# Kernel tuning notes

Hardware: AMD Instinct MI355X
Metric: run time of the kernel (lower is better)

## Reference

```python
import jax, jax.numpy as jnp
import numpy as np

B, S, H = 8, 1024, 1536          # batch, seq, hidden_size
NH, HD, AH = 8, 96, 768          # heads after head_ratio=2, head_size=hidden/16, all_head_size
K = 7                            # conv_kernel_size
IM = 3072                        # intermediate_size
EPS = 1e-12                      # ConvBert layer_norm_eps


def _ln(x, g, b):
    m = x.mean(-1, keepdims=True)
    v = ((x - m) ** 2).mean(-1, keepdims=True)
    return (x - m) / jnp.sqrt(v + EPS) * g + b


def _windows(x, k):
    # x: [B,S,C] -> sliding windows [B,S,k,C] with 'same' padding ((k-1)//2 each side, k odd)
    p = (k - 1) // 2
    xp = jnp.pad(x, ((0, 0), (p, p), (0, 0)))
    idx = jnp.arange(x.shape[1])[:, None] + jnp.arange(k)[None, :]
    return xp[:, idx, :]


def _forward(embed, wq, bq, wk, bk, wv, bv, dw, pw, sep_b, wck, bck, wco, bco,
             wso, bso, ln1_g, ln1_b, wi, bi, wo, bo, ln2_g, ln2_b, wd, bd):
    b, s, _ = embed.shape
    # --- projections (weights stored [in,out]) ---
    q = embed @ wq + bq            # [B,S,AH]
    kk = embed @ wk + bk
    v = embed @ wv + bv
    # --- SeparableConv1D on hidden states: depthwise(k=7) then pointwise + bias ---
    win_h = _windows(embed, K)                             # [B,S,K,H]
    dconv = jnp.einsum('bskc,ck->bsc', win_h, dw)          # depthwise, [B,S,H]
    sep = dconv @ pw + sep_b                               # pointwise, [B,S,AH]
    # --- span dynamic conv kernels ---
    conv_attn = sep * q                                    # [B,S,AH]
    ck = (conv_attn @ wck + bck).reshape(b, s, NH, K)      # [B,S,NH,K]
    ck = jax.nn.softmax(ck, axis=-1)
    co = embed @ wco + bco                                 # [B,S,AH]
    win_co = _windows(co, K).reshape(b, s, K, NH, HD)      # [B,S,K,NH,HD]
    conv_out = jnp.einsum('bskhd,bshk->bshd', win_co, ck)  # [B,S,NH,HD]
    # --- standard self-attention on the reduced heads ---
    qh = q.reshape(b, s, NH, HD)
    kh = kk.reshape(b, s, NH, HD)
    vh = v.reshape(b, s, NH, HD)
    scores = jnp.einsum('bqhd,bkhd->bhqk', qh, kh) / jnp.sqrt(jnp.float32(HD))
    probs = jax.nn.softmax(scores, axis=-1)
    ctx = jnp.einsum('bhqk,bkhd->bqhd', probs, vh)         # [B,S,NH,HD]
    # --- concat attention heads with conv heads -> [B,S,2*NH,HD] -> [B,S,H] ---
    ctx = jnp.concatenate([ctx, conv_out], axis=2).reshape(b, s, H)
    # --- self output (dropout is identity at inference) ---
    attn_out = _ln(ctx @ wso + bso + embed, ln1_g, ln1_b)
    # --- FFN ---
    inter = jax.nn.gelu(attn_out @ wi + bi, approximate=False)
    layer_out = _ln(inter @ wo + bo + attn_out, ln2_g, ln2_b)
    # --- global max pooling over sequence + linear decoder ---
    pooled = layer_out.max(axis=1)                         # [B,H]
    logits = pooled @ wd + bd                              # [B,1]
    return logits


def setup_inputs() -> dict:
    key = jax.random.key(0)
    ks = jax.random.split(key, 32)
    rn = lambda i, shape, s=0.02: jax.random.normal(ks[i], shape, jnp.float32) * s
    d = {}
    d['embed'] = jax.random.normal(ks[0], (B, S, H), jnp.float32)
    d['wq'] = rn(1, (H, AH)); d['bq'] = jnp.zeros((AH,), jnp.float32)
    d['wk'] = rn(2, (H, AH)); d['bk'] = jnp.zeros((AH,), jnp.float32)
    d['wv'] = rn(3, (H, AH)); d['bv'] = jnp.zeros((AH,), jnp.float32)
    d['dw'] = rn(4, (H, K)); d['pw'] = rn(5, (H, AH)); d['sep_b'] = jnp.zeros((AH,), jnp.float32)
    d['wck'] = rn(6, (AH, NH * K)); d['bck'] = jnp.zeros((NH * K,), jnp.float32)
    d['wco'] = rn(7, (H, AH)); d['bco'] = jnp.zeros((AH,), jnp.float32)
    d['wso'] = rn(8, (H, H)); d['bso'] = jnp.zeros((H,), jnp.float32)
    d['ln1_g'] = jnp.ones((H,), jnp.float32); d['ln1_b'] = jnp.zeros((H,), jnp.float32)
    d['wi'] = rn(9, (H, IM)); d['bi'] = jnp.zeros((IM,), jnp.float32)
    d['wo'] = rn(10, (IM, H)); d['bo'] = jnp.zeros((H,), jnp.float32)
    d['ln2_g'] = jnp.ones((H,), jnp.float32); d['ln2_b'] = jnp.zeros((H,), jnp.float32)
    d['wd'] = jax.random.uniform(ks[11], (H, 1), jnp.float32, -0.1, 0.1)
    d['bd'] = jnp.zeros((1,), jnp.float32)
    return d


def reference(embed, wq, bq, wk, bk, wv, bv, dw, pw, sep_b, wck, bck, wco, bco,
              wso, bso, ln1_g, ln1_b, wi, bi, wo, bo, ln2_g, ln2_b, wd, bd):
    return _forward(embed, wq, bq, wk, bk, wv, bv, dw, pw, sep_b, wck, bck, wco, bco,
                    wso, bso, ln1_g, ln1_b, wi, bi, wo, bo, ln2_g, ln2_b, wd, bd)
```

## Files before the change

kernel.cpp:

```cpp
#include <hip/hip_runtime.h>


typedef __bf16 bf16_t;
typedef short s16x8 __attribute__((ext_vector_type(8)));
typedef float f32x4 __attribute__((ext_vector_type(4)));

#define BB  8
#define SS  1024
#define HH  1536
#define NHH 8
#define HDD 96
#define AHH 768
#define IMM 3072

__device__ __forceinline__ float rd_adapt(const void* p, long long i, int isbf) {
    return isbf ? (float)((const bf16_t*)p)[i] : ((const float*)p)[i];
}
__device__ __forceinline__ float bs2f(short x) {
    return __uint_as_float(((unsigned)(unsigned short)x) << 16);
}
__device__ __forceinline__ short f2bs(float f) {
    bf16_t b = (bf16_t)f; short s; __builtin_memcpy(&s, &b, 2); return s;
}

__device__ __forceinline__ float gelu_f(float v) {
    float u = v * (0.7978845608f + 0.0356774081f * v * v);
    float e = __expf(2.0f * u);
    float t = 1.0f - 2.0f / (e + 1.0f);
    return 0.5f * v * (1.0f + t);
}

__device__ __forceinline__ void gl2lds16(const bf16_t* g, bf16_t* l) {
    __builtin_amdgcn_global_load_lds(
        (__attribute__((address_space(1))) const void*)g,
        (__attribute__((address_space(3))) void*)l, 16, 0, 0);
}

#define FENCE() asm volatile("" ::: "memory")
#define BARRIER() do { FENCE(); __builtin_amdgcn_s_barrier(); FENCE(); } while (0)
#define LGKM(n) asm volatile("s_waitcnt lgkmcnt(" #n ")" ::: "memory")
#define VMCNT(n) asm volatile("s_waitcnt vmcnt(" #n ")" ::: "memory")
#define SCHEDB() __builtin_amdgcn_sched_barrier(0)
#define PRIO(n) __builtin_amdgcn_s_setprio(n)
#define RDV(base, imm) (*(const s16x8*)(smb + (base) + (imm)))

#define MFMA_CLUSTER(AF, BF, IO, JO)                                            \
    _Pragma("unroll")                                                           \
    for (int i_ = 0; i_ < 4; i_++)                                              \
        _Pragma("unroll")                                                       \
        for (int j_ = 0; j_ < 2; j_++) {                                        \
            acc[(IO)+i_][(JO)+j_] = __builtin_amdgcn_mfma_f32_16x16x32_bf16(    \
                AF[i_][0], BF[j_][0], acc[(IO)+i_][(JO)+j_], 0, 0, 0);          \
            acc[(IO)+i_][(JO)+j_] = __builtin_amdgcn_mfma_f32_16x16x32_bf16(    \
                AF[i_][1], BF[j_][1], acc[(IO)+i_][(JO)+j_], 0, 0, 0);          \
        }

__global__ __launch_bounds__(256)
void detect_kernel(const void* __restrict__ embed, int* __restrict__ flag)
{
    __shared__ int cnt[256];
    int t = threadIdx.x;
    float x = (float)((const bf16_t*)embed)[t];
    float a = fabsf(x);
    cnt[t] = (a > 1e-3f && a < 50.0f) ? 1 : 0;
    __syncthreads();
    for (int o = 128; o > 0; o >>= 1) { if (t < o) cnt[t] += cnt[t + o]; __syncthreads(); }
    if (t == 0) *flag = (cnt[0] >= 205) ? 1 : 0;
}

__global__ __launch_bounds__(256)
void convert_embed(const void* __restrict__ in, bf16_t* __restrict__ out,
                   const int* __restrict__ flagp)
{
    int isbf = *flagp;
    long long i0 = ((long long)blockIdx.x * 256 + threadIdx.x) * 8;
    if (isbf) {
        *(s16x8*)(out + i0) = *(const s16x8*)((const bf16_t*)in + i0);
    } else {
        const float* f = (const float*)in;
        #pragma unroll
        for (int j = 0; j < 8; j++) out[i0 + j] = (bf16_t)f[i0 + j];
    }
}

__global__ __launch_bounds__(256)
void concat_bias(const void* __restrict__ b0, const void* __restrict__ b1,
                 const void* __restrict__ b2, const void* __restrict__ b3,
                 bf16_t* __restrict__ out, const int* __restrict__ flagp)
{
    int isbf = *flagp;
    int t = blockIdx.x * 256 + threadIdx.x;
    int sel = t / 768, off = t - sel * 768;
    const void* src = (sel == 0) ? b0 : (sel == 1) ? b1 : (sel == 2) ? b2 : b3;
    out[t] = (bf16_t)rd_adapt(src, off, isbf);
}

__global__ __launch_bounds__(256)
void dw_transpose(const void* __restrict__ dw, float* __restrict__ dwT,
                  const int* __restrict__ flagp)
{
    int isbf = *flagp;
    int i = blockIdx.x * 256 + threadIdx.x;
    if (i >= 7 * HH) return;
    int k = i % 7, c = i / 7;
    dwT[k * HH + c] = rd_adapt(dw, (long long)c * 7 + k, isbf);
}

template<int IB, int OB>
__device__ __forceinline__ void tile_step(
    char* smb, int vA0, int vA1, int vB0, int vB1,
    const char* gA00, const char* gA01, const char* gA10, const char* gA11,
    const char* gB00, const char* gB01, const char* gB10, const char* gB11,
    char* ldsAw, char* ldsBw, int k1, int k2,
    s16x8 (&af0)[4][2], s16x8 (&af1)[4][2],
    s16x8 (&bf0)[2][2], s16x8 (&bf1)[2][2],
    f32x4 (&acc)[8][4])
{
    BARRIER();
    bf1[0][0] = RDV(vB0, IB + 4096); bf1[0][1] = RDV(vB1, IB + 4096);
    bf1[1][0] = RDV(vB0, IB + 6144); bf1[1][1] = RDV(vB1, IB + 6144);
    gl2lds16((const bf16_t*)(gA10 + k1), (bf16_t*)(ldsAw + OB + 16384));
    gl2lds16((const bf16_t*)(gA11 + k1), (bf16_t*)(ldsAw + OB + 17408));
    LGKM(4); SCHEDB(); PRIO(1);
    MFMA_CLUSTER(af0, bf0, 0, 0);
    PRIO(0);

    BARRIER();
    af1[0][0] = RDV(vA0, IB + 8192);  af1[0][1] = RDV(vA1, IB + 8192);
    af1[1][0] = RDV(vA0, IB + 10240); af1[1][1] = RDV(vA1, IB + 10240);
    af1[2][0] = RDV(vA0, IB + 12288); af1[2][1] = RDV(vA1, IB + 12288);
    af1[3][0] = RDV(vA0, IB + 14336); af1[3][1] = RDV(vA1, IB + 14336);
    gl2lds16((const bf16_t*)(gB10 + k1), (bf16_t*)(ldsBw + OB + 16384));
    gl2lds16((const bf16_t*)(gB11 + k1), (bf16_t*)(ldsBw + OB + 17408));
    LGKM(8); SCHEDB(); PRIO(1);
    MFMA_CLUSTER(af0, bf1, 0, 2);
    PRIO(0);

    BARRIER();
    gl2lds16((const bf16_t*)(gB00 + k2), (bf16_t*)(ldsBw + IB));
    gl2lds16((const bf16_t*)(gB01 + k2), (bf16_t*)(ldsBw + IB + 1024));
    gl2lds16((const bf16_t*)(gA00 + k2), (bf16_t*)(ldsAw + IB));
    gl2lds16((const bf16_t*)(gA01 + k2), (bf16_t*)(ldsAw + IB + 1024));
    LGKM(0); SCHEDB(); PRIO(1);
    MFMA_CLUSTER(af1, bf1, 4, 2);
    PRIO(0);

    VMCNT(4);
    BARRIER();
    af0[0][0] = RDV(vA0, OB + 0);    af0[0][1] = RDV(vA1, OB + 0);
    af0[1][0] = RDV(vA0, OB + 2048); af0[1][1] = RDV(vA1, OB + 2048);
    af0[2][0] = RDV(vA0, OB + 4096); af0[2][1] = RDV(vA1, OB + 4096);
    af0[3][0] = RDV(vA0, OB + 6144); af0[3][1] = RDV(vA1, OB + 6144);
    PRIO(1);
    MFMA_CLUSTER(af1, bf0, 4, 0);
    PRIO(0);
    bf0[0][0] = RDV(vB0, OB + 0);    bf0[0][1] = RDV(vB1, OB + 0);
    bf0[1][0] = RDV(vB0, OB + 2048); bf0[1][1] = RDV(vB1, OB + 2048);
}

__global__ __launch_bounds__(512, 2)
void gemm256(const bf16_t* __restrict__ A, const bf16_t* __restrict__ Bt,
             bf16_t* __restrict__ C, const void* __restrict__ bias,
             const bf16_t* __restrict__ emul, int lde, const int* __restrict__ flagp,
             int M, int N, int Kd, int lda, int ldb, int ldc, int act, int tilesN)
{
    __shared__ bf16_t Sm[65536];
    char* smb = (char*)Sm;
    int isbf = flagp ? *flagp : 1;

    int nwg = gridDim.x;
    int orig = blockIdx.x;
    int q = nwg >> 3, r = nwg & 7;
    int xcd = orig & 7, lid = orig >> 3;
    int wg = (xcd < r ? xcd * (q + 1) : r * (q + 1) + (xcd - r) * q) + lid;
    int row0 = (wg / tilesN) * 256;
    int col0 = (wg % tilesN) * 256;

    int tid = threadIdx.x;
    int wave = tid >> 6, lane = tid & 63;
    int wm = wave >> 2, wn = wave & 3;
    int lm = lane & 15, kq = lane >> 4;

    int srow = lane >> 3;
    int scol = 8 * ((lane & 7) ^ srow);

    const char* gA00 = (const char*)(A + (long long)(row0 +   0 + (2*wave + 0)*8 + srow) * lda + scol);
    const char* gA01 = (const char*)(A + (long long)(row0 +   0 + (2*wave + 1)*8 + srow) * lda + scol);
    const char* gA10 = (const char*)(A + (long long)(row0 + 128 + (2*wave + 0)*8 + srow) * lda + scol);
    const char* gA11 = (const char*)(A + (long long)(row0 + 128 + (2*wave + 1)*8 + srow) * lda + scol);
    const char* gB00 = (const char*)(Bt + (long long)(col0 +   0 + (2*wave + 0)*8 + srow) * ldb + scol);
    const char* gB01 = (const char*)(Bt + (long long)(col0 +   0 + (2*wave + 1)*8 + srow) * ldb + scol);
    const char* gB10 = (const char*)(Bt + (long long)(col0 + 128 + (2*wave + 0)*8 + srow) * ldb + scol);
    const char* gB11 = (const char*)(Bt + (long long)(col0 + 128 + (2*wave + 1)*8 + srow) * ldb + scol);

    char* ldsAw = smb + 2 * wave * 1024;
    char* ldsBw = smb + 65536 + 2 * wave * 1024;

    int xo = (lm & 7) << 4;
    int c0 = (kq * 16) ^ xo;
    int c1 = (64 + kq * 16) ^ xo;
    int vA0 = (wm * 128 + lm) * 128 + c0;
    int vA1 = (wm * 128 + lm) * 128 + c1;
    int vB0 = 65536 + (wn * 64 + lm) * 128 + c0;
    int vB1 = 65536 + (wn * 64 + lm) * 128 + c1;

    f32x4 acc[8][4] = {};
    s16x8 af0[4][2], af1[4][2], bf0[2][2], bf1[2][2];

    int KT = Kd >> 6;
    int KTm1 = KT - 1;

    gl2lds16((const bf16_t*)gA00, (bf16_t*)(ldsAw));
    gl2lds16((const bf16_t*)gA01, (bf16_t*)(ldsAw + 1024));
    gl2lds16((const bf16_t*)gA10, (bf16_t*)(ldsAw + 16384));
    gl2lds16((const bf16_t*)gA11, (bf16_t*)(ldsAw + 17408));
    gl2lds16((const bf16_t*)gB00, (bf16_t*)(ldsBw));
    gl2lds16((const bf16_t*)gB01, (bf16_t*)(ldsBw + 1024));
    gl2lds16((const bf16_t*)gB10, (bf16_t*)(ldsBw + 16384));
    gl2lds16((const bf16_t*)gB11, (bf16_t*)(ldsBw + 17408));
    int kb1 = min(1, KTm1) << 7;
    gl2lds16((const bf16_t*)(gB00 + kb1), (bf16_t*)(ldsBw + 32768));
    gl2lds16((const bf16_t*)(gB01 + kb1), (bf16_t*)(ldsBw + 33792));
    gl2lds16((const bf16_t*)(gA00 + kb1), (bf16_t*)(ldsAw + 32768));
    gl2lds16((const bf16_t*)(gA01 + kb1), (bf16_t*)(ldsAw + 33792));
    VMCNT(4);
    BARRIER();
    af0[0][0] = RDV(vA0, 0);    af0[0][1] = RDV(vA1, 0);
    af0[1][0] = RDV(vA0, 2048); af0[1][1] = RDV(vA1, 2048);
    af0[2][0] = RDV(vA0, 4096); af0[2][1] = RDV(vA1, 4096);
    af0[3][0] = RDV(vA0, 6144); af0[3][1] = RDV(vA1, 6144);
    bf0[0][0] = RDV(vB0, 0);    bf0[0][1] = RDV(vB1, 0);
    bf0[1][0] = RDV(vB0, 2048); bf0[1][1] = RDV(vB1, 2048);

    for (int it = 0; it < (KT >> 1); ++it) {
        int t = it << 1;
        int k1 = min(t + 1, KTm1) << 7;
        int k2 = min(t + 2, KTm1) << 7;
        int k3 = min(t + 3, KTm1) << 7;
        tile_step<0, 32768>(smb, vA0, vA1, vB0, vB1,
                            gA00, gA01, gA10, gA11, gB00, gB01, gB10, gB11,
                            ldsAw, ldsBw, k1, k2, af0, af1, bf0, bf1, acc);
        tile_step<32768, 0>(smb, vA0, vA1, vB0, vB1,
                            gA00, gA01, gA10, gA11, gB00, gB01, gB10, gB11,
                            ldsAw, ldsBw, k2, k3, af0, af1, bf0, bf1, acc);
    }

    #pragma unroll
    for (int j = 0; j < 4; j++) {
        int gcol = col0 + wn * 64 + j * 16 + lm;
        float bv = bias ? rd_adapt(bias, gcol, isbf) : 0.0f;
        #pragma unroll
        for (int ip = 0; ip < 8; ip++) {
            int grow0 = row0 + wm * 128 + ip * 16 + kq * 4;
            #pragma unroll
            for (int r = 0; r < 4; r++) {
                float v = acc[ip][j][r] + bv;
                if (emul) v *= (float)emul[(long long)(grow0 + r) * lde + gcol];
                if (act) v = gelu_f(v);
                C[(long long)(grow0 + r) * ldc + gcol] = (bf16_t)v;
            }
        }
    }
}

__global__ __launch_bounds__(256)
void gemm_tile(const bf16_t* __restrict__ A, const bf16_t* __restrict__ Bt,
               bf16_t* __restrict__ C, const void* __restrict__ bias, long long biasOff,
               const bf16_t* __restrict__ emul, int lde, const int* __restrict__ flagp,
               int M, int N, int Kd, int lda, int ldb, int ldc,
               float scale, int act, int beta, int nlim)
{
    __shared__ bf16_t Sm[16384];

    int isbf = flagp ? *flagp : 1;
    int tid  = threadIdx.x;
    int wave = tid >> 6, lane = tid & 63;
    int wm = wave >> 1, wn = wave & 1;
    int row0 = blockIdx.x * 128;
    int col0 = blockIdx.y * 128;
    int lm = lane & 15;
    int kq = lane >> 4;

    int sr = tid >> 2;
    int sc = (tid & 3) * 8;
    const bf16_t* ga0 = A + (long long)(row0 + sr) * lda + sc;
    const bf16_t* ga1 = A + (long long)(row0 + 64 + sr) * lda + sc;
    int br0 = min(col0 + sr, nlim);
    int br1 = min(col0 + 64 + sr, nlim);
    const bf16_t* gb0 = Bt + (long long)br0 * ldb + sc;
    const bf16_t* gb1 = Bt + (long long)br1 * ldb + sc;
    bf16_t* lw = Sm + wave * 512;

    f32x4 acc[4][4] = {};

    for (int k0 = 0; k0 < Kd; k0 += 64) {
        #pragma unroll
        for (int h = 0; h < 2; h++) {
            int kh = k0 + h * 32;
            gl2lds16(ga0 + kh, lw + h * 4096);
            gl2lds16(ga1 + kh, lw + h * 4096 + 2048);
            gl2lds16(gb0 + kh, lw + 8192 + h * 4096);
            gl2lds16(gb1 + kh, lw + 8192 + h * 4096 + 2048);
        }
        __syncthreads();

        s16x8 af[2][4], bfr[2][4];
        #pragma unroll
        for (int h = 0; h < 2; h++) {
            #pragma unroll
            for (int i = 0; i < 4; i++)
                af[h][i] = *(const s16x8*)(Sm + h * 4096 + (wm * 64 + i * 16 + lm) * 32 + kq * 8);
            #pragma unroll
            for (int j = 0; j < 4; j++)
                bfr[h][j] = *(const s16x8*)(Sm + 8192 + h * 4096 + (wn * 64 + j * 16 + lm) * 32 + kq * 8);
        }
        #pragma unroll
        for (int i = 0; i < 4; i++)
            #pragma unroll
            for (int j = 0; j < 4; j++) {
                acc[i][j] = __builtin_amdgcn_mfma_f32_16x16x32_bf16(af[0][i], bfr[0][j], acc[i][j], 0, 0, 0);
                acc[i][j] = __builtin_amdgcn_mfma_f32_16x16x32_bf16(af[1][i], bfr[1][j], acc[i][j], 0, 0, 0);
            }
        __syncthreads();
    }

    #pragma unroll
    for (int j = 0; j < 4; j++) {
        int gcol = col0 + wn * 64 + j * 16 + lm;
        if (gcol >= N) continue;
        float bv = bias ? rd_adapt(bias, biasOff + gcol, isbf) : 0.0f;
        #pragma unroll
        for (int i = 0; i < 4; i++) {
            int grow0 = row0 + wm * 64 + i * 16 + kq * 4;
            #pragma unroll
            for (int r = 0; r < 4; r++) {
                float v = acc[i][j][r] * scale + bv;
                long long ci = (long long)(grow0 + r) * ldc + gcol;
                if (beta) v += (float)C[ci];
                if (emul) v *= (float)emul[(long long)(grow0 + r) * lde + gcol];
                if (act) v = gelu_f(v);
                C[ci] = (bf16_t)v;
            }
        }
    }
}

__global__ __launch_bounds__(256, 2)
void flash_attn(const bf16_t* __restrict__ qkv, const bf16_t* __restrict__ vT,
                bf16_t* __restrict__ ctxcat)
{
    const float ascale = 0.1020620726159658f;
    __shared__ bf16_t KL[12288];
    __shared__ bf16_t Pl[4 * 32 * 136];

    int bh = blockIdx.x;
    int b = bh >> 3, h = bh & 7;
    const bf16_t* Qp = qkv  + (long long)b * SS * 3072 + h * HDD;
    const bf16_t* Kp = qkv  + (long long)b * SS * 3072 + 768 + h * HDD;
    const bf16_t* Vt = vT   + (long long)b * AHH * SS + (long long)h * HDD * SS;
    bf16_t*       Op = ctxcat + (long long)b * SS * HH + h * HDD;

    int tid = threadIdx.x, wave = tid >> 6, lane = tid & 63;
    int lm = lane & 15, kq = lane >> 4;
    int q0 = blockIdx.y * 128 + wave * 32;
    bf16_t* Pw = Pl + wave * 32 * 136;

    int srow_l = lane >> 2;
    int sslot  = ((lane & 3) ^ ((lane >> 3) & 3)) * 8;
    auto stageK = [&](int kt) {
        #pragma unroll
        for (int i = 0; i < 6; i++) {
            int qc = wave + 4 * i;
            int fb = qc >> 3, cc = qc & 7;
            gl2lds16(Kp + (long long)(kt * 128 + cc * 16 + srow_l) * 3072 + fb * 32 + sslot,
                     KL + qc * 512);
        }
    };
    const char* klb = (const char*)KL + lm * 64 + ((kq ^ ((lm >> 1) & 3)) << 4);

    s16x8 aq[2][3];
    #pragma unroll
    for (int i = 0; i < 2; i++)
        #pragma unroll
        for (int kf = 0; kf < 3; kf++)
            aq[i][kf] = *(const s16x8*)(Qp + (long long)(q0 + i * 16 + lm) * 3072 + kf * 32 + kq * 8);

    stageK(0);
    __syncthreads();

    f32x4 Oacc[2][6] = {};
    float mrow[2][4], lrow[2][4];
    #pragma unroll
    for (int i = 0; i < 2; i++)
        #pragma unroll
        for (int r = 0; r < 4; r++) { mrow[i][r] = -1e30f; lrow[i][r] = 0.0f; }

    for (int kt = 0; kt < 8; kt++) {
        f32x4 S[2][8] = {};
        #pragma unroll
        for (int j = 0; j < 8; j++) {
            s16x8 bk[3];
            #pragma unroll
            for (int kf = 0; kf < 3; kf++)
                bk[kf] = *(const s16x8*)(klb + kf * 8192 + j * 1024);
            #pragma unroll
            for (int i = 0; i < 2; i++)
                #pragma unroll
                for (int kf = 0; kf < 3; kf++)
                    S[i][j] = __builtin_amdgcn_mfma_f32_16x16x32_bf16(aq[i][kf], bk[kf], S[i][j], 0, 0, 0);
        }
        __syncthreads();
        if (kt < 7) stageK(kt + 1);

        float mnew[2][4];
        #pragma unroll
        for (int i = 0; i < 2; i++) {
            #pragma unroll
            for (int r = 0; r < 4; r++) {
                float mx = -1e30f;
                #pragma unroll
                for (int j = 0; j < 8; j++) mx = fmaxf(mx, S[i][j][r]);
                #pragma unroll
                for (int msk = 1; msk <= 8; msk <<= 1) mx = fmaxf(mx, __shfl_xor(mx, msk));
                mnew[i][r] = fmaxf(mrow[i][r], mx * ascale);
            }
        }
        #pragma unroll
        for (int i = 0; i < 2; i++) {
            #pragma unroll
            for (int r = 0; r < 4; r++) {
                float al = __expf(mrow[i][r] - mnew[i][r]);
                lrow[i][r] *= al;
                #pragma unroll
                for (int n = 0; n < 6; n++) Oacc[i][n][r] *= al;
                mrow[i][r] = mnew[i][r];
            }
        }
        float psum[2][4] = {};
        #pragma unroll
        for (int i = 0; i < 2; i++) {
            #pragma unroll
            for (int j = 0; j < 8; j++) {
                #pragma unroll
                for (int r = 0; r < 4; r++) {
                    float p = __expf(S[i][j][r] * ascale - mnew[i][r]);
                    psum[i][r] += p;
                    Pw[(i * 16 + kq * 4 + r) * 136 + j * 16 + lm] = (bf16_t)p;
                }
            }
        }
        #pragma unroll
        for (int i = 0; i < 2; i++) {
            #pragma unroll
            for (int r = 0; r < 4; r++) {
                float t = psum[i][r];
                #pragma unroll
                for (int msk = 1; msk <= 8; msk <<= 1) t += __shfl_xor(t, msk);
                lrow[i][r] += t;
            }
        }

        s16x8 ap[2][4];
        #pragma unroll
        for (int i = 0; i < 2; i++)
            #pragma unroll
            for (int kf = 0; kf < 4; kf++)
                ap[i][kf] = *(const s16x8*)(Pw + (i * 16 + lm) * 136 + kf * 32 + kq * 8);
        #pragma unroll
        for (int n = 0; n < 6; n++) {
            s16x8 bv[4];
            #pragma unroll
            for (int kf = 0; kf < 4; kf++)
                bv[kf] = *(const s16x8*)(Vt + (long long)(n * 16 + lm) * SS + kt * 128 + kf * 32 + kq * 8);
            #pragma unroll
            for (int i = 0; i < 2; i++)
                #pragma unroll
                for (int kf = 0; kf < 4; kf++)
                    Oacc[i][n] = __builtin_amdgcn_mfma_f32_16x16x32_bf16(ap[i][kf], bv[kf], Oacc[i][n], 0, 0, 0);
        }
        __syncthreads();
    }

    #pragma unroll
    for (int i = 0; i < 2; i++) {
        #pragma unroll
        for (int n = 0; n < 6; n++) {
            #pragma unroll
            for (int r = 0; r < 4; r++) {
                int row = q0 + i * 16 + kq * 4 + r;
                int col = n * 16 + lm;
                Op[(long long)row * HH + col] = (bf16_t)(Oacc[i][n][r] / lrow[i][r]);
            }
        }
    }
}

__global__ __launch_bounds__(256)
void transpose_v8(const void* __restrict__ in, bf16_t* __restrict__ out,
                  int R, int C, int ldin, long long inOff,
                  long long sInB, long long sOutB, const int* __restrict__ flagp)
{
    __shared__ bf16_t t[64][72];
    int isbf = flagp ? *flagp : 1;
    int z = blockIdx.z;
    long long base = inOff + (long long)z * sInB;
    bf16_t* op = out + (long long)z * sOutB;
    int cb = blockIdx.x * 64, rb = blockIdx.y * 64;
    int tr = threadIdx.x >> 3;
    int tc = (threadIdx.x & 7) * 8;
    #pragma unroll
    for (int it = 0; it < 2; it++) {
        int r = tr + it * 32;
        int gc = cb + tc;
        if (isbf && gc + 8 <= C) {
            *(s16x8*)&t[r][tc] =
                *(const s16x8*)((const bf16_t*)in + base + (long long)(rb + r) * ldin + gc);
        } else {
            #pragma unroll
            for (int j = 0; j < 8; j++)
                t[r][tc + j] = (gc + j < C)
                    ? (bf16_t)rd_adapt(in, base + (long long)(rb + r) * ldin + gc + j, isbf)
                    : (bf16_t)0.0f;
        }
    }
    __syncthreads();
    int oc = threadIdx.x >> 2;
    int r0 = (threadIdx.x & 3) * 16;
    s16x8 v0, v1;
    #pragma unroll
    for (int j = 0; j < 8; j++) v0[j] = f2bs(bs2f(*(short*)&t[r0 + j][oc]));
    #pragma unroll
    for (int j = 0; j < 8; j++) v1[j] = f2bs(bs2f(*(short*)&t[r0 + 8 + j][oc]));
    bf16_t* dst = op + (long long)(cb + oc) * R + rb + r0;
    *(s16x8*)dst = v0;
    *(s16x8*)(dst + 8) = v1;
}

__global__ __launch_bounds__(256)
void transpose_pad4(const void* __restrict__ i0, const void* __restrict__ i1,
                    const void* __restrict__ i2, const void* __restrict__ i3,
                    bf16_t* __restrict__ out, const int* __restrict__ flagp)
{
    __shared__ bf16_t t[64][72];
    int isbf = *flagp;
    int z = blockIdx.z;
    const void* in = (z == 0) ? i0 : (z == 1) ? i1 : (z == 2) ? i2 : i3;
    bf16_t* op = out + (long long)z * (768ll * 1536);
    int cb = blockIdx.x * 64, rb = blockIdx.y * 64;
    int tr = threadIdx.x >> 3;
    int tc = (threadIdx.x & 7) * 8;
    #pragma unroll
    for (int it = 0; it < 2; it++) {
        int r = tr + it * 32;
        if (isbf) {
            *(s16x8*)&t[r][tc] =
                *(const s16x8*)((const bf16_t*)in + (long long)(rb + r) * 768 + cb + tc);
        } else {
            #pragma unroll
            for (int j = 0; j < 8; j++)
                t[r][tc + j] = (bf16_t)rd_adapt(in, (long long)(rb + r) * 768 + cb + tc + j, isbf);
        }
    }
    __syncthreads();
    int oc = threadIdx.x >> 2;
    int r0 = (threadIdx.x & 3) * 16;
    s16x8 v0, v1;
    #pragma unroll
    for (int j = 0; j < 8; j++) v0[j] = *(short*)&t[r0 + j][oc];
    #pragma unroll
    for (int j = 0; j < 8; j++) v1[j] = *(short*)&t[r0 + 8 + j][oc];
    bf16_t* dst = op + (long long)(cb + oc) * 1536 + rb + r0;
    *(s16x8*)dst = v0;
    *(s16x8*)(dst + 8) = v1;
}

__global__ __launch_bounds__(256)
void dconv_kernel(const bf16_t* __restrict__ ebuf, const float* __restrict__ dwT,
                  bf16_t* __restrict__ out)
{
    long long i = (long long)blockIdx.x * 256 + threadIdx.x;
    int c8 = (int)(i % 192) * 8;
    long long bs = i / 192;
    int s = (int)(bs % SS);
    float acc[8] = {};
    #pragma unroll
    for (int k = 0; k < 7; k++) {
        int ss = s + k - 3;
        if (ss < 0 || ss >= SS) continue;
        s16x8 v = *(const s16x8*)(ebuf + (bs + (k - 3)) * HH + c8);
        const float4* wp = (const float4*)(dwT + k * HH + c8);
        float4 w0 = wp[0], w1 = wp[1];
        acc[0] += bs2f(v[0]) * w0.x; acc[1] += bs2f(v[1]) * w0.y;
        acc[2] += bs2f(v[2]) * w0.z; acc[3] += bs2f(v[3]) * w0.w;
        acc[4] += bs2f(v[4]) * w1.x; acc[5] += bs2f(v[5]) * w1.y;
        acc[6] += bs2f(v[6]) * w1.z; acc[7] += bs2f(v[7]) * w1.w;
    }
    s16x8 o;
    #pragma unroll
    for (int j = 0; j < 8; j++) o[j] = f2bs(acc[j]);
    *(s16x8*)(out + bs * HH + c8) = o;
}

__global__ __launch_bounds__(256)
void ck_softmax(const bf16_t* __restrict__ ck, float* __restrict__ ckp)
{
    int i = blockIdx.x * 256 + threadIdx.x;
    if (i >= BB * SS * NHH) return;
    int h = i % NHH;
    long long bs = i / NHH;
    const bf16_t* src = ck + bs * 64 + h * 7;
    float v[7], mx = -1e30f;
    #pragma unroll
    for (int k = 0; k < 7; k++) { v[k] = (float)src[k]; mx = fmaxf(mx, v[k]); }
    float sum = 0.0f;
    #pragma unroll
    for (int k = 0; k < 7; k++) { v[k] = expf(v[k] - mx); sum += v[k]; }
    float inv = 1.0f / sum;
    float* dst = ckp + bs * 56 + h * 7;
    #pragma unroll
    for (int k = 0; k < 7; k++) dst[k] = v[k] * inv;
}

__global__ __launch_bounds__(256)
void conv_out_kernel(const bf16_t* __restrict__ co, int ldco,
                     const float* __restrict__ ckp, bf16_t* __restrict__ ctxcat)
{
    long long i = (long long)blockIdx.x * 256 + threadIdx.x;
    int ch = (int)(i % 96);
    long long bs = i / 96;
    int s = (int)(bs % SS);
    int hd0 = ch * 8;
    int h = hd0 / HDD;
    const float* w = ckp + bs * 56 + h * 7;
    float wk[7];
    #pragma unroll
    for (int k = 0; k < 7; k++) wk[k] = w[k];
    float acc[8] = {};
    #pragma unroll
    for (int k = 0; k < 7; k++) {
        int ss = s + k - 3;
        if (ss < 0 || ss >= SS) continue;
        s16x8 v = *(const s16x8*)(co + (bs + (k - 3)) * ldco + hd0);
        #pragma unroll
        for (int j = 0; j < 8; j++) acc[j] += bs2f(v[j]) * wk[k];
    }
    s16x8 o;
    #pragma unroll
    for (int j = 0; j < 8; j++) o[j] = f2bs(acc[j]);
    *(s16x8*)(ctxcat + bs * HH + AHH + hd0) = o;
}

__global__ __launch_bounds__(192)
void ln_kernel(const bf16_t* __restrict__ y, const bf16_t* __restrict__ res,
               const void* __restrict__ g, const void* __restrict__ bta,
               bf16_t* __restrict__ outb, const int* __restrict__ flagp)
{
    int isbf = *flagp;
    long long row = blockIdx.x;
    int tid = threadIdx.x;
    int c0 = tid * 8;
    s16x8 vy = *(const s16x8*)(y + row * HH + c0);
    s16x8 vr = *(const s16x8*)(res + row * HH + c0);
    float x[8], s = 0.0f, s2 = 0.0f;
    #pragma unroll
    for (int j = 0; j < 8; j++) {
        float v = bs2f(vy[j]) + bs2f(vr[j]);
        x[j] = v; s += v; s2 += v * v;
    }
    #pragma unroll
    for (int o = 32; o > 0; o >>= 1) { s += __shfl_down(s, o); s2 += __shfl_down(s2, o); }
    __shared__ float w1[3], w2[3];
    int lane = tid & 63, wv = tid >> 6;
    if (lane == 0) { w1[wv] = s; w2[wv] = s2; }
    __syncthreads();
    float S1 = w1[0] + w1[1] + w1[2];
    float S2 = w2[0] + w2[1] + w2[2];
    float mean = S1 * (1.0f / HH);
    float var  = S2 * (1.0f / HH) - mean * mean;
    float inv  = rsqrtf(var + 1e-12f);
    s16x8 o;
    #pragma unroll
    for (int j = 0; j < 8; j++) {
        float v = (x[j] - mean) * inv * rd_adapt(g, c0 + j, isbf) + rd_adapt(bta, c0 + j, isbf);
        o[j] = f2bs(v);
    }
    *(s16x8*)(outb + row * HH + c0) = o;
}

__global__ __launch_bounds__(192)
void maxpool_p1(const bf16_t* __restrict__ lo, float* __restrict__ part)
{
    int sc = blockIdx.x, b = blockIdx.y;
    int tid = threadIdx.x;
    int c0 = tid * 8;
    const bf16_t* p = lo + ((long long)b * SS + sc * 32) * HH + c0;
    float m[8];
    #pragma unroll
    for (int j = 0; j < 8; j++) m[j] = -1e30f;
    for (int r = 0; r < 32; r++) {
        s16x8 v = *(const s16x8*)(p + (long long)r * HH);
        #pragma unroll
        for (int j = 0; j < 8; j++) m[j] = fmaxf(m[j], bs2f(v[j]));
    }
    float* dst = part + ((long long)b * 32 + sc) * HH + c0;
    *(float4*)(dst)     = make_float4(m[0], m[1], m[2], m[3]);
    *(float4*)(dst + 4) = make_float4(m[4], m[5], m[6], m[7]);
}

__global__ __launch_bounds__(192)
void pool_decode(const float* __restrict__ part, const void* __restrict__ wd,
                 const void* __restrict__ bd, void* __restrict__ out,
                 const int* __restrict__ flagp)
{
    int isbf = *flagp;
    int b = blockIdx.x;
    int tid = threadIdx.x;
    int c0 = tid * 8;
    float m[8];
    #pragma unroll
    for (int j = 0; j < 8; j++) m[j] = -1e30f;
    for (int ch = 0; ch < 32; ch++) {
        const float4* q = (const float4*)(part + ((long long)b * 32 + ch) * HH + c0);
        float4 a = q[0], c = q[1];
        m[0] = fmaxf(m[0], a.x); m[1] = fmaxf(m[1], a.y);
        m[2] = fmaxf(m[2], a.z); m[3] = fmaxf(m[3], a.w);
        m[4] = fmaxf(m[4], c.x); m[5] = fmaxf(m[5], c.y);
        m[6] = fmaxf(m[6], c.z); m[7] = fmaxf(m[7], c.w);
    }
    float s = 0.0f;
    #pragma unroll
    for (int j = 0; j < 8; j++) s += m[j] * rd_adapt(wd, c0 + j, isbf);
    #pragma unroll
    for (int o = 32; o > 0; o >>= 1) s += __shfl_down(s, o);
    __shared__ float sa[3];
    int lane = tid & 63, wv = tid >> 6;
    if (lane == 0) sa[wv] = s;
    __syncthreads();
    if (tid == 0) {
        float r = sa[0] + sa[1] + sa[2] + rd_adapt(bd, 0, isbf);
        if (isbf) ((bf16_t*)out)[b] = (bf16_t)r;
        else      ((float*)out)[b]  = r;
    }
}

extern "C" void kernel_launch(void* const* d_in, const int* in_sizes, int n_in,
                              void* d_out, int out_size, void* d_ws, size_t ws_size,
                              hipStream_t stream)
{
    const void* embed = d_in[0];
    const void* wq  = d_in[1];  const void* bq  = d_in[2];
    const void* wk  = d_in[3];  const void* bk  = d_in[4];
    const void* wv  = d_in[5];  const void* bv  = d_in[6];
    const void* dw  = d_in[7];  const void* pw  = d_in[8];  const void* sep_b = d_in[9];
    const void* wck = d_in[10]; const void* bck = d_in[11];
    const void* wco = d_in[12]; const void* bco = d_in[13];
    const void* wso = d_in[14]; const void* bso = d_in[15];
    const void* ln1g = d_in[16]; const void* ln1b = d_in[17];
    const void* wi  = d_in[18]; const void* bi  = d_in[19];
    const void* wo  = d_in[20]; const void* bo  = d_in[21];
    const void* ln2g = d_in[22]; const void* ln2b = d_in[23];
    const void* wd  = d_in[24]; const void* bd  = d_in[25];
    (void)ws_size; (void)in_sizes; (void)n_in; (void)out_size;

    char* ws = (char*)d_ws;
    char* A  = ws;
    char* B  = ws + 50331648;
    char* C_ = ws + 75497472;
    char* D  = ws + 88080384;
    char* E  = ws + 113246208;
    char* F  = ws + 138412032;
    char* XP = ws + 143130624;

    bf16_t* qkvco  = (bf16_t*)A;
    bf16_t* ybuf   = (bf16_t*)A;
    bf16_t* interb = (bf16_t*)A;
    bf16_t* lout   = (bf16_t*)A;
    bf16_t* wT_all = (bf16_t*)B;
    bf16_t* dconvb = (bf16_t*)B;
    bf16_t* ckb    = (bf16_t*)B;
    float*  ckp    = (float*)(B + 1310720);
    bf16_t* vT     = (bf16_t*)B;
    bf16_t* wfT    = (bf16_t*)B;
    bf16_t* sepb   = (bf16_t*)C_;
    float*  mpart  = (float*)C_;
    bf16_t* ctxcat = (bf16_t*)D;
    bf16_t* attn   = (bf16_t*)D;
    bf16_t* ebuf   = (bf16_t*)E;
    bf16_t* y2     = (bf16_t*)E;
    bf16_t* wT     = (bf16_t*)F;
    int*    flag   = (int*)XP;
    bf16_t* cbias  = (bf16_t*)(XP + 256);
    float*  dwT    = (float*)(XP + 8192);

    dim3 blk(256);

    auto gemm_big = [&](const bf16_t* Ai, const bf16_t* Bt, bf16_t* Ci, const void* bias,
                        const bf16_t* emul, int lde, const int* fl,
                        int M, int N, int Kd, int lda, int ldb, int ldc, int act) {
        int tn = N / 256;
        dim3 g((M / 256) * tn);
        gemm256<<<g, dim3(512), 0, stream>>>(Ai, Bt, Ci, bias, emul, lde, fl,
                                             M, N, Kd, lda, ldb, ldc, act, tn);
    };
    auto gemm = [&](const bf16_t* Ai, const bf16_t* Bt, bf16_t* Ci, const void* bias,
                    long long biasOff, const bf16_t* emul, int lde, const int* fl,
                    int M, int N, int Kd, int lda, int ldb, int ldc,
                    float scale, int act, int beta, int nlim) {
        dim3 g(M / 128, (N + 127) / 128, 1);
        gemm_tile<<<g, blk, 0, stream>>>(Ai, Bt, Ci, bias, biasOff, emul, lde, fl,
                                         M, N, Kd, lda, ldb, ldc,
                                         scale, act, beta, nlim);
    };
    auto transpose = [&](const void* in, bf16_t* out, int R, int Cc, int Cpad, int ldin,
                         long long inOff, int batch, long long sInB, long long sOutB,
                         const int* fl) {
        dim3 g(Cpad / 64, R / 64, batch);
        transpose_v8<<<g, blk, 0, stream>>>(in, out, R, Cc, ldin, inOff, sInB, sOutB, fl);
    };

    detect_kernel<<<dim3(1), blk, 0, stream>>>(embed, flag);
    convert_embed<<<dim3(6144), blk, 0, stream>>>(embed, ebuf, flag);

    transpose_pad4<<<dim3(12, 24, 4), blk, 0, stream>>>(wq, wk, wv, wco, wT_all, flag);
    concat_bias<<<dim3(12), blk, 0, stream>>>(bq, bk, bv, bco, cbias, flag);
    gemm_big(ebuf, wT_all, qkvco, cbias, nullptr, 0, nullptr,
             8192, 3072, 1536, HH, HH, 3072, 0);

    dw_transpose<<<dim3(42), blk, 0, stream>>>(dw, dwT, flag);
    dconv_kernel<<<dim3((BB * SS * 192) / 256), blk, 0, stream>>>(ebuf, dwT, dconvb);
    transpose(pw, wT, 1536, 768, 768, 768, 0, 1, 0, 0, flag);
    gemm(dconvb, wT, sepb, sep_b, 0, qkvco, 3072, flag,
         8192, 768, 1536, HH, HH, AHH, 1.0f, 0, 0, 767);

    transpose(wck, wT, 768, 56, 128, 56, 0, 1, 0, 0, flag);
    gemm(sepb, wT, ckb, bck, 0, nullptr, 0, flag,
         8192, 56, 768, AHH, AHH, 64, 1.0f, 0, 0, 127);
    ck_softmax<<<dim3((BB * SS * NHH) / 256), blk, 0, stream>>>(ckb, ckp);
    conv_out_kernel<<<dim3((BB * SS * 96) / 256), blk, 0, stream>>>(qkvco + 2304, 3072, ckp, ctxcat);

    transpose(qkvco, vT, 1024, 768, 768, 3072, 1536, 8, 1024ll * 3072, 768ll * 1024, nullptr);
    flash_attn<<<dim3(64, 8), blk, 0, stream>>>(qkvco, vT, ctxcat);

    transpose(wso, wT, 1536, 1536, 1536, 1536, 0, 1, 0, 0, flag);
    gemm_big(ctxcat, wT, ybuf, bso, nullptr, 0, flag,
             8192, 1536, 1536, HH, HH, HH, 0);
    ln_kernel<<<dim3(8192), dim3(192), 0, stream>>>(ybuf, ebuf, ln1g, ln1b, attn, flag);

    transpose(wi, wfT, 1536, 3072, 3072, 3072, 0, 1, 0, 0, flag);
    gemm_big(attn, wfT, interb, bi, nullptr, 0, flag,
             8192, 3072, 1536, HH, HH, IMM, 1);
    transpose(wo, wfT, 3072, 1536, 1536, 1536, 0, 1, 0, 0, flag);
    gemm_big(interb, wfT, y2, bo, nullptr, 0, flag,
             8192, 1536, 3072, IMM, IMM, HH, 0);
    ln_kernel<<<dim3(8192), dim3(192), 0, stream>>>(y2, attn, ln2g, ln2b, lout, flag);

    maxpool_p1<<<dim3(32, 8), dim3(192), 0, stream>>>(lout, mpart);
    pool_decode<<<dim3(BB), dim3(192), 0, stream>>>(mpart, wd, bd, d_out, flag);
}
```

Before: 847.2 us.

## Batch weight prep into two kernels, fuse softmax and residual adds

```diff
diff --git a/kernel.cpp b/kernel.cpp
--- a/kernel.cpp
+++ b/kernel.cpp
@@ -83,27 +83,96 @@
     }
 }
 
+__device__ __forceinline__ void tr64_body(const void* in, bf16_t* out,
+                                          int C, int ldin, int R,
+                                          int cb, int rb, int isbf,
+                                          bf16_t (*t)[72])
+{
+    int tr = threadIdx.x >> 3;
+    int tc = (threadIdx.x & 7) * 8;
+    #pragma unroll
+    for (int it = 0; it < 2; it++) {
+        int r = tr + it * 32;
+        int gc = cb + tc;
+        if (isbf && gc + 8 <= C) {
+            *(s16x8*)&t[r][tc] =
+                *(const s16x8*)((const bf16_t*)in + (long long)(rb + r) * ldin + gc);
+        } else {
+            #pragma unroll
+            for (int j = 0; j < 8; j++)
+                t[r][tc + j] = (gc + j < C)
+                    ? (bf16_t)rd_adapt(in, (long long)(rb + r) * ldin + gc + j, isbf)
+                    : (bf16_t)0.0f;
+        }
+    }
+    __syncthreads();
+    int oc = threadIdx.x >> 2;
+    int r0 = (threadIdx.x & 3) * 16;
+    s16x8 v0, v1;
+    #pragma unroll
+    for (int j = 0; j < 8; j++) v0[j] = *(short*)&t[r0 + j][oc];
+    #pragma unroll
+    for (int j = 0; j < 8; j++) v1[j] = *(short*)&t[r0 + 8 + j][oc];
+    bf16_t* dst = out + (long long)(cb + oc) * R + rb + r0;
+    *(s16x8*)dst = v0;
+    *(s16x8*)(dst + 8) = v1;
+}
+
 __global__ __launch_bounds__(256)
-void concat_bias(const void* __restrict__ b0, const void* __restrict__ b1,
-                 const void* __restrict__ b2, const void* __restrict__ b3,
-                 bf16_t* __restrict__ out, const int* __restrict__ flagp)
-{
+void prep_weights(const void* __restrict__ wq, const void* __restrict__ wk,
+                  const void* __restrict__ wv, const void* __restrict__ wco,
+                  const void* __restrict__ pw, const void* __restrict__ wck,
+                  const void* __restrict__ dw,
+                  const void* __restrict__ b0, const void* __restrict__ b1,
+                  const void* __restrict__ b2, const void* __restrict__ b3,
+                  bf16_t* __restrict__ wT_all, bf16_t* __restrict__ pwT,
+                  bf16_t* __restrict__ wckT, float* __restrict__ dwT,
+                  bf16_t* __restrict__ cbias, const int* __restrict__ flagp)
+{
+    __shared__ bf16_t t[64][72];
     int isbf = *flagp;
-    int t = blockIdx.x * 256 + threadIdx.x;
-    int sel = t / 768, off = t - sel * 768;
-    const void* src = (sel == 0) ? b0 : (sel == 1) ? b1 : (sel == 2) ? b2 : b3;
-    out[t] = (bf16_t)rd_adapt(src, off, isbf);
+    int j = blockIdx.x;
+    if (j < 1152) {
+        int z = j / 288, rm = j % 288;
+        const void* in = (z == 0) ? wq : (z == 1) ? wk : (z == 2) ? wv : wco;
+        tr64_body(in, wT_all + (long long)z * 768 * 1536, 768, 768, 1536,
+                  (rm % 12) * 64, (rm / 12) * 64, isbf, t);
+    } else if (j < 1440) {
+        int rm = j - 1152;
+        tr64_body(pw, pwT, 768, 768, 1536, (rm % 12) * 64, (rm / 12) * 64, isbf, t);
+    } else if (j < 1464) {
+        int rm = j - 1440;
+        tr64_body(wck, wckT, 56, 56, 768, (rm % 2) * 64, (rm / 2) * 64, isbf, t);
+    } else if (j < 1506) {
+        int idx = (j - 1464) * 256 + threadIdx.x;
+        int k = idx % 7, c = idx / 7;
+        dwT[k * HH + c] = rd_adapt(dw, (long long)c * 7 + k, isbf);
+    } else {
+        int tt = (j - 1506) * 256 + threadIdx.x;
+        int sel = tt / 768, off = tt - sel * 768;
+        const void* src = (sel == 0) ? b0 : (sel == 1) ? b1 : (sel == 2) ? b2 : b3;
+        cbias[tt] = (bf16_t)rd_adapt(src, off, isbf);
+    }
 }
 
 __global__ __launch_bounds__(256)
-void dw_transpose(const void* __restrict__ dw, float* __restrict__ dwT,
-                  const int* __restrict__ flagp)
-{
+void prep_late(const void* __restrict__ wso, const void* __restrict__ wi,
+               const void* __restrict__ wo, bf16_t* __restrict__ wsoT,
+               bf16_t* __restrict__ wiT, bf16_t* __restrict__ woT,
+               const int* __restrict__ flagp)
+{
+    __shared__ bf16_t t[64][72];
     int isbf = *flagp;
-    int i = blockIdx.x * 256 + threadIdx.x;
-    if (i >= 7 * HH) return;
-    int k = i % 7, c = i / 7;
-    dwT[k * HH + c] = rd_adapt(dw, (long long)c * 7 + k, isbf);
+    int j = blockIdx.x;
+    if (j < 576) {
+        tr64_body(wso, wsoT, 1536, 1536, 1536, (j % 24) * 64, (j / 24) * 64, isbf, t);
+    } else if (j < 1728) {
+        int rm = j - 576;
+        tr64_body(wi, wiT, 3072, 3072, 1536, (rm % 48) * 64, (rm / 48) * 64, isbf, t);
+    } else {
+        int rm = j - 1728;
+        tr64_body(wo, woT, 1536, 1536, 3072, (rm % 24) * 64, (rm / 24) * 64, isbf, t);
+    }
 }
 
 template<int IB, int OB>
@@ -161,6 +230,7 @@
 __global__ __launch_bounds__(512, 2)
 void gemm256(const bf16_t* __restrict__ A, const bf16_t* __restrict__ Bt,
              bf16_t* __restrict__ C, const void* __restrict__ bias,
+             const bf16_t* __restrict__ resi, int ldr,
              const bf16_t* __restrict__ emul, int lde, const int* __restrict__ flagp,
              int M, int N, int Kd, int lda, int ldb, int ldc, int act, int tilesN)
 {
@@ -255,6 +325,7 @@
             #pragma unroll
             for (int r = 0; r < 4; r++) {
                 float v = acc[ip][j][r] + bv;
+                if (resi) v += (float)resi[(long long)(grow0 + r) * ldr + gcol];
                 if (emul) v *= (float)emul[(long long)(grow0 + r) * lde + gcol];
                 if (act) v = gelu_f(v);
                 C[(long long)(grow0 + r) * ldc + gcol] = (bf16_t)v;
@@ -528,48 +599,10 @@
     int r0 = (threadIdx.x & 3) * 16;
     s16x8 v0, v1;
     #pragma unroll
-    for (int j = 0; j < 8; j++) v0[j] = f2bs(bs2f(*(short*)&t[r0 + j][oc]));
-    #pragma unroll
-    for (int j = 0; j < 8; j++) v1[j] = f2bs(bs2f(*(short*)&t[r0 + 8 + j][oc]));
+    for (int j = 0; j < 8; j++) v0[j] = *(short*)&t[r0 + j][oc];
+    #pragma unroll
+    for (int j = 0; j < 8; j++) v1[j] = *(short*)&t[r0 + 8 + j][oc];
     bf16_t* dst = op + (long long)(cb + oc) * R + rb + r0;
-    *(s16x8*)dst = v0;
-    *(s16x8*)(dst + 8) = v1;
-}
-
-__global__ __launch_bounds__(256)
-void transpose_pad4(const void* __restrict__ i0, const void* __restrict__ i1,
-                    const void* __restrict__ i2, const void* __restrict__ i3,
-                    bf16_t* __restrict__ out, const int* __restrict__ flagp)
-{
-    __shared__ bf16_t t[64][72];
-    int isbf = *flagp;
-    int z = blockIdx.z;
-    const void* in = (z == 0) ? i0 : (z == 1) ? i1 : (z == 2) ? i2 : i3;
-    bf16_t* op = out + (long long)z * (768ll * 1536);
-    int cb = blockIdx.x * 64, rb = blockIdx.y * 64;
-    int tr = threadIdx.x >> 3;
-    int tc = (threadIdx.x & 7) * 8;
-    #pragma unroll
-    for (int it = 0; it < 2; it++) {
-        int r = tr + it * 32;
-        if (isbf) {
-            *(s16x8*)&t[r][tc] =
-                *(const s16x8*)((const bf16_t*)in + (long long)(rb + r) * 768 + cb + tc);
-        } else {
-            #pragma unroll
-            for (int j = 0; j < 8; j++)
-                t[r][tc + j] = (bf16_t)rd_adapt(in, (long long)(rb + r) * 768 + cb + tc + j, isbf);
-        }
-    }
-    __syncthreads();
-    int oc = threadIdx.x >> 2;
-    int r0 = (threadIdx.x & 3) * 16;
-    s16x8 v0, v1;
-    #pragma unroll
-    for (int j = 0; j < 8; j++) v0[j] = *(short*)&t[r0 + j][oc];
-    #pragma unroll
-    for (int j = 0; j < 8; j++) v1[j] = *(short*)&t[r0 + 8 + j][oc];
-    bf16_t* dst = op + (long long)(cb + oc) * 1536 + rb + r0;
     *(s16x8*)dst = v0;
     *(s16x8*)(dst + 8) = v1;
 }
@@ -602,28 +635,8 @@
 }
 
 __global__ __launch_bounds__(256)
-void ck_softmax(const bf16_t* __restrict__ ck, float* __restrict__ ckp)
-{
-    int i = blockIdx.x * 256 + threadIdx.x;
-    if (i >= BB * SS * NHH) return;
-    int h = i % NHH;
-    long long bs = i / NHH;
-    const bf16_t* src = ck + bs * 64 + h * 7;
-    float v[7], mx = -1e30f;
-    #pragma unroll
-    for (int k = 0; k < 7; k++) { v[k] = (float)src[k]; mx = fmaxf(mx, v[k]); }
-    float sum = 0.0f;
-    #pragma unroll
-    for (int k = 0; k < 7; k++) { v[k] = expf(v[k] - mx); sum += v[k]; }
-    float inv = 1.0f / sum;
-    float* dst = ckp + bs * 56 + h * 7;
-    #pragma unroll
-    for (int k = 0; k < 7; k++) dst[k] = v[k] * inv;
-}
-
-__global__ __launch_bounds__(256)
 void conv_out_kernel(const bf16_t* __restrict__ co, int ldco,
-                     const float* __restrict__ ckp, bf16_t* __restrict__ ctxcat)
+                     const bf16_t* __restrict__ ckb, bf16_t* __restrict__ ctxcat)
 {
     long long i = (long long)blockIdx.x * 256 + threadIdx.x;
     int ch = (int)(i % 96);
@@ -631,10 +644,17 @@
     int s = (int)(bs % SS);
     int hd0 = ch * 8;
     int h = hd0 / HDD;
-    const float* w = ckp + bs * 56 + h * 7;
-    float wk[7];
-    #pragma unroll
-    for (int k = 0; k < 7; k++) wk[k] = w[k];
+    const bf16_t* src = ckb + bs * 64 + h * 7;
+    float wk[7], mx = -1e30f;
+    #pragma unroll
+    for (int k = 0; k < 7; k++) { wk[k] = (float)src[k]; mx = fmaxf(mx, wk[k]); }
+    float sum = 0.0f;
+    #pragma unroll
+    for (int k = 0; k < 7; k++) { wk[k] = expf(wk[k] - mx); sum += wk[k]; }
+    float inv = 1.0f / sum;
+    #pragma unroll
+    for (int k = 0; k < 7; k++) wk[k] *= inv;
+
     float acc[8] = {};
     #pragma unroll
     for (int k = 0; k < 7; k++) {
@@ -651,7 +671,7 @@
 }
 
 __global__ __launch_bounds__(192)
-void ln_kernel(const bf16_t* __restrict__ y, const bf16_t* __restrict__ res,
+void ln_kernel(const bf16_t* __restrict__ y,
                const void* __restrict__ g, const void* __restrict__ bta,
                bf16_t* __restrict__ outb, const int* __restrict__ flagp)
 {
@@ -660,11 +680,10 @@
     int tid = threadIdx.x;
     int c0 = tid * 8;
     s16x8 vy = *(const s16x8*)(y + row * HH + c0);
-    s16x8 vr = *(const s16x8*)(res + row * HH + c0);
     float x[8], s = 0.0f, s2 = 0.0f;
     #pragma unroll
     for (int j = 0; j < 8; j++) {
-        float v = bs2f(vy[j]) + bs2f(vr[j]);
+        float v = bs2f(vy[j]);
         x[j] = v; s += v; s2 += v * v;
     }
     #pragma unroll
@@ -778,16 +797,18 @@
     bf16_t* wT_all = (bf16_t*)B;
     bf16_t* dconvb = (bf16_t*)B;
     bf16_t* ckb    = (bf16_t*)B;
-    float*  ckp    = (float*)(B + 1310720);
     bf16_t* vT     = (bf16_t*)B;
-    bf16_t* wfT    = (bf16_t*)B;
+    bf16_t* wiT    = (bf16_t*)B;
+    bf16_t* woT    = (bf16_t*)(B + 9437184);
     bf16_t* sepb   = (bf16_t*)C_;
     float*  mpart  = (float*)C_;
     bf16_t* ctxcat = (bf16_t*)D;
     bf16_t* attn   = (bf16_t*)D;
     bf16_t* ebuf   = (bf16_t*)E;
     bf16_t* y2     = (bf16_t*)E;
-    bf16_t* wT     = (bf16_t*)F;
+    bf16_t* pwT    = (bf16_t*)F;
+    bf16_t* wckT   = (bf16_t*)(F + 2359296);
+    bf16_t* wsoT   = (bf16_t*)F;
     int*    flag   = (int*)XP;
     bf16_t* cbias  = (bf16_t*)(XP + 256);
     float*  dwT    = (float*)(XP + 8192);
@@ -795,11 +816,12 @@
     dim3 blk(256);
 
     auto gemm_big = [&](const bf16_t* Ai, const bf16_t* Bt, bf16_t* Ci, const void* bias,
-                        const bf16_t* emul, int lde, const int* fl,
-                        int M, int N, int Kd, int lda, int ldb, int ldc, int act) {
+                        const bf16_t* resi, int ldr, const bf16_t* emul, int lde,
+                        const int* fl, int M, int N, int Kd, int lda, int ldb, int ldc,
+                        int act) {
         int tn = N / 256;
         dim3 g((M / 256) * tn);
-        gemm256<<<g, dim3(512), 0, stream>>>(Ai, Bt, Ci, bias, emul, lde, fl,
+        gemm256<<<g, dim3(512), 0, stream>>>(Ai, Bt, Ci, bias, resi, ldr, emul, lde, fl,
                                              M, N, Kd, lda, ldb, ldc, act, tn);
     };
     auto gemm = [&](const bf16_t* Ai, const bf16_t* Bt, bf16_t* Ci, const void* bias,
@@ -811,48 +833,39 @@
                                          M, N, Kd, lda, ldb, ldc,
                                          scale, act, beta, nlim);
     };
-    auto transpose = [&](const void* in, bf16_t* out, int R, int Cc, int Cpad, int ldin,
-                         long long inOff, int batch, long long sInB, long long sOutB,
-                         const int* fl) {
-        dim3 g(Cpad / 64, R / 64, batch);
-        transpose_v8<<<g, blk, 0, stream>>>(in, out, R, Cc, ldin, inOff, sInB, sOutB, fl);
-    };
 
     detect_kernel<<<dim3(1), blk, 0, stream>>>(embed, flag);
+    prep_weights<<<dim3(1518), blk, 0, stream>>>(wq, wk, wv, wco, pw, wck, dw,
+                                                 bq, bk, bv, bco,
+                                                 wT_all, pwT, wckT, dwT, cbias, flag);
     convert_embed<<<dim3(6144), blk, 0, stream>>>(embed, ebuf, flag);
 
-    transpose_pad4<<<dim3(12, 24, 4), blk, 0, stream>>>(wq, wk, wv, wco, wT_all, flag);
-    concat_bias<<<dim3(12), blk, 0, stream>>>(bq, bk, bv, bco, cbias, flag);
-    gemm_big(ebuf, wT_all, qkvco, cbias, nullptr, 0, nullptr,
+    gemm_big(ebuf, wT_all, qkvco, cbias, nullptr, 0, nullptr, 0, nullptr,
              8192, 3072, 1536, HH, HH, 3072, 0);
 
-    dw_transpose<<<dim3(42), blk, 0, stream>>>(dw, dwT, flag);
     dconv_kernel<<<dim3((BB * SS * 192) / 256), blk, 0, stream>>>(ebuf, dwT, dconvb);
-    transpose(pw, wT, 1536, 768, 768, 768, 0, 1, 0, 0, flag);
-    gemm(dconvb, wT, sepb, sep_b, 0, qkvco, 3072, flag,
+    gemm(dconvb, pwT, sepb, sep_b, 0, qkvco, 3072, flag,
          8192, 768, 1536, HH, HH, AHH, 1.0f, 0, 0, 767);
 
-    transpose(wck, wT, 768, 56, 128, 56, 0, 1, 0, 0, flag);
-    gemm(sepb, wT, ckb, bck, 0, nullptr, 0, flag,
+    gemm(sepb, wckT, ckb, bck, 0, nullptr, 0, flag,
          8192, 56, 768, AHH, AHH, 64, 1.0f, 0, 0, 127);
-    ck_softmax<<<dim3((BB * SS * NHH) / 256), blk, 0, stream>>>(ckb, ckp);
-    conv_out_kernel<<<dim3((BB * SS * 96) / 256), blk, 0, stream>>>(qkvco + 2304, 3072, ckp, ctxcat);
-
-    transpose(qkvco, vT, 1024, 768, 768, 3072, 1536, 8, 1024ll * 3072, 768ll * 1024, nullptr);
+    conv_out_kernel<<<dim3((BB * SS * 96) / 256), blk, 0, stream>>>(qkvco + 2304, 3072, ckb, ctxcat);
+
+    transpose_v8<<<dim3(12, 16, 8), blk, 0, stream>>>(qkvco, vT, 1024, 768, 3072, 1536,
+                                                      1024ll * 3072, 768ll * 1024, nullptr);
     flash_attn<<<dim3(64, 8), blk, 0, stream>>>(qkvco, vT, ctxcat);
 
-    transpose(wso, wT, 1536, 1536, 1536, 1536, 0, 1, 0, 0, flag);
-    gemm_big(ctxcat, wT, ybuf, bso, nullptr, 0, flag,
+    prep_late<<<dim3(2880), blk, 0, stream>>>(wso, wi, wo, wsoT, wiT, woT, flag);
+
+    gemm_big(ctxcat, wsoT, ybuf, bso, ebuf, HH, nullptr, 0, flag,
              8192, 1536, 1536, HH, HH, HH, 0);
-    ln_kernel<<<dim3(8192), dim3(192), 0, stream>>>(ybuf, ebuf, ln1g, ln1b, attn, flag);
-
-    transpose(wi, wfT, 1536, 3072, 3072, 3072, 0, 1, 0, 0, flag);
-    gemm_big(attn, wfT, interb, bi, nullptr, 0, flag,
+    ln_kernel<<<dim3(8192), dim3(192), 0, stream>>>(ybuf, ln1g, ln1b, attn, flag);
+
+    gemm_big(attn, wiT, interb, bi, nullptr, 0, nullptr, 0, flag,
              8192, 3072, 1536, HH, HH, IMM, 1);
-    transpose(wo, wfT, 3072, 1536, 1536, 1536, 0, 1, 0, 0, flag);
-    gemm_big(interb, wfT, y2, bo, nullptr, 0, flag,
+    gemm_big(interb, woT, y2, bo, attn, HH, nullptr, 0, flag,
              8192, 1536, 3072, IMM, IMM, HH, 0);
-    ln_kernel<<<dim3(8192), dim3(192), 0, stream>>>(y2, attn, ln2g, ln2b, lout, flag);
+    ln_kernel<<<dim3(8192), dim3(192), 0, stream>>>(y2, ln2g, ln2b, lout, flag);
 
     maxpool_p1<<<dim3(32, 8), dim3(192), 0, stream>>>(lout, mpart);
     pool_decode<<<dim3(BB), dim3(192), 0, stream>>>(mpart, wd, bd, d_out, flag);
```

Measured after the change: 878.5 us. +3.7%, slower.
